# Kernel tuning notes

Hardware: AMD Instinct MI355X
Metric: run time of the kernel (lower is better)

## Reference

```python
import jax, jax.numpy as jnp
import numpy as np

STRIDES = [8, 16, 32, 64, 128]
SIZES = [32.0, 64.0, 128.0, 256.0, 512.0]
FEAT_HW = [(100, 152), (50, 76), (25, 38), (13, 19), (7, 10)]
N, C, A, K = 2, 256, 9, 80
SCORE_TH, TOPK, NMS_TH, MAX_DET = 0.05, 1000, 0.5, 100
IMG_H, IMG_W = 800.0, 1216.0
SCALE_CLAMP = float(np.log(1000.0 / 16.0))


def _cell_anchors(size):
    ratios = [0.5, 1.0, 2.0]
    scales = [2 ** 0, 2 ** (1.0 / 3), 2 ** (2.0 / 3)]
    out = []
    for s in scales:
        area = (size * s) ** 2
        for r in ratios:
            w = np.sqrt(area / r)
            h = w * r
            out.append([-w / 2.0, -h / 2.0, w / 2.0, h / 2.0])
    return np.asarray(out, np.float32)  # (9, 4)


def make_anchors():
    ancs = []
    for (H, W), st, sz in zip(FEAT_HW, STRIDES, SIZES):
        cell = _cell_anchors(sz)
        sx = np.arange(W, dtype=np.float32) * st
        sy = np.arange(H, dtype=np.float32) * st
        gx, gy = np.meshgrid(sx, sy)
        shifts = np.stack([gx.ravel(), gy.ravel(), gx.ravel(), gy.ravel()], 1)
        ancs.append((shifts[:, None, :] + cell[None, :, :]).reshape(-1, 4).astype(np.float32))
    return ancs


def setup_inputs() -> dict:
    key = jax.random.key(0)
    ks = jax.random.split(key, 10)
    inp = {}
    for i, (H, W) in enumerate(FEAT_HW):
        inp[f"feat{i}"] = jax.random.normal(ks[i], (N, C, H, W), jnp.float32)
    inp["cls_sub_w"] = jax.random.normal(ks[5], (4, C, C, 3, 3), jnp.float32) * 0.01
    inp["cls_sub_b"] = jnp.zeros((4, C), jnp.float32)
    inp["bbox_sub_w"] = jax.random.normal(ks[6], (4, C, C, 3, 3), jnp.float32) * 0.01
    inp["bbox_sub_b"] = jnp.zeros((4, C), jnp.float32)
    inp["cls_score_w"] = jax.random.normal(ks[7], (A * K, C, 3, 3), jnp.float32) * 0.1
    inp["cls_score_b"] = jnp.full((A * K,), float(-np.log((1 - 0.01) / 0.01)), jnp.float32)
    inp["bbox_pred_w"] = jax.random.normal(ks[8], (A * 4, C, 3, 3), jnp.float32) * 0.01
    inp["bbox_pred_b"] = jnp.zeros((A * 4,), jnp.float32)
    for i, a in enumerate(make_anchors()):
        inp[f"anc{i}"] = jnp.asarray(a)
    return inp


def conv3(x, w, b):
    y = jax.lax.conv_general_dilated(x, w, (1, 1), 'SAME',
                                     dimension_numbers=('NCHW', 'OIHW', 'NCHW'))
    return y + b[None, :, None, None]


def head_level(x, csw, csb, bsw, bsb, scw, scb, bpw, bpb):
    c = x
    r = x
    for i in range(4):
        c = jax.nn.relu(conv3(c, csw[i], csb[i]))
        r = jax.nn.relu(conv3(r, bsw[i], bsb[i]))
    return conv3(c, scw, scb), conv3(r, bpw, bpb)


def to_NHWA_K(t, k):
    n, _, h, w = t.shape
    return t.reshape(n, -1, k, h, w).transpose(0, 3, 4, 1, 2).reshape(n, -1, k)


def decode(deltas, anchors):
    wa = anchors[..., 2] - anchors[..., 0]
    ha = anchors[..., 3] - anchors[..., 1]
    xa = anchors[..., 0] + 0.5 * wa
    ya = anchors[..., 1] + 0.5 * ha
    dx, dy = deltas[..., 0], deltas[..., 1]
    dw = jnp.minimum(deltas[..., 2], SCALE_CLAMP)
    dh = jnp.minimum(deltas[..., 3], SCALE_CLAMP)
    cx = dx * wa + xa
    cy = dy * ha + ya
    w = jnp.exp(dw) * wa
    h = jnp.exp(dh) * ha
    return jnp.stack([cx - 0.5 * w, cy - 0.5 * h, cx + 0.5 * w, cy + 0.5 * h], -1)


def iou_vs_all(box, boxes):
    lt = jnp.maximum(box[:2], boxes[:, :2])
    rb = jnp.minimum(box[2:], boxes[:, 2:])
    wh = jnp.clip(rb - lt, 0.0)
    inter = wh[:, 0] * wh[:, 1]
    a1 = (box[2] - box[0]) * (box[3] - box[1])
    a2 = (boxes[:, 2] - boxes[:, 0]) * (boxes[:, 3] - boxes[:, 1])
    return inter / (a1 + a2 - inter + 1e-9)


def nms_image(boxes, scores, classes):
    # class-aware NMS via coordinate offset per class (batched_nms trick)
    off = classes.astype(boxes.dtype)[:, None] * 4096.0
    b = boxes + off

    def body(i, st):
        sc, bi, bs = st
        j = jnp.argmax(sc)
        s = sc[j]
        bi = bi.at[i].set(j)
        bs = bs.at[i].set(s)
        iou = iou_vs_all(b[j], b)
        sc = jnp.where(iou > NMS_TH, 0.0, sc).at[j].set(0.0)
        return (sc, bi, bs)

    bi0 = jnp.zeros((MAX_DET,), jnp.int32)
    bs0 = jnp.zeros((MAX_DET,), boxes.dtype)
    _, bi, bs = jax.lax.fori_loop(0, MAX_DET, body, (scores, bi0, bs0))
    return boxes[bi], bs, classes[bi]


def reference(feat0, feat1, feat2, feat3, feat4, cls_sub_w, cls_sub_b,
              bbox_sub_w, bbox_sub_b, cls_score_w, cls_score_b,
              bbox_pred_w, bbox_pred_b, anc0, anc1, anc2, anc3, anc4):
    feats = [feat0, feat1, feat2, feat3, feat4]
    ancs = [anc0, anc1, anc2, anc3, anc4]
    cand_b, cand_s, cand_c = [], [], []
    for f, anc in zip(feats, ancs):
        logits, deltas = head_level(f, cls_sub_w, cls_sub_b, bbox_sub_w, bbox_sub_b,
                                    cls_score_w, cls_score_b, bbox_pred_w, bbox_pred_b)
        cls = to_NHWA_K(logits, K)       # (N, HWA, K)
        reg = to_NHWA_K(deltas, 4)       # (N, HWA, 4)
        n, hwa, _ = reg.shape
        prob = jax.nn.sigmoid(cls.reshape(n, hwa * K))
        ntk = min(TOPK, hwa)             # d2: min(topk_candidates, box_reg_i.size(0))
        vals, idxs = jax.lax.top_k(prob, ntk)
        a_idx = idxs // K
        c_idx = idxs % K
        d = jnp.take_along_axis(reg, a_idx[..., None], axis=1)   # (N, ntk, 4)
        anc_sel = anc[a_idx]                                      # (N, ntk, 4)
        boxes = decode(d, anc_sel)
        boxes = jnp.stack([jnp.clip(boxes[..., 0], 0.0, IMG_W),
                           jnp.clip(boxes[..., 1], 0.0, IMG_H),
                           jnp.clip(boxes[..., 2], 0.0, IMG_W),
                           jnp.clip(boxes[..., 3], 0.0, IMG_H)], -1)
        scores = jnp.where(vals > SCORE_TH, vals, 0.0)  # score threshold (keep_idxs)
        cand_b.append(boxes)
        cand_s.append(scores)
        cand_c.append(c_idx)
    B = jnp.concatenate(cand_b, 1)
    S = jnp.concatenate(cand_s, 1)
    Cl = jnp.concatenate(cand_c, 1)
    det_boxes, det_scores, det_classes = jax.vmap(nms_image)(B, S, Cl)
    return det_boxes, det_scores, det_classes
```

## Files before the change

### kernel.cpp

```cpp
#include <hip/hip_runtime.h>
#include <math.h>

#define NIMG 2
#define NCAND 4630
#define MAXDET 100
#define IMG_W_F 1216.0f
#define IMG_H_F 800.0f
#define SCORE_THR 0.05f
#define NMS_THR 0.5f
#define SCALE_CLAMP_F 4.135166556742356f

typedef __attribute__((ext_vector_type(8))) _Float16 f16x8;
typedef __attribute__((ext_vector_type(16))) float f32x16;

#define WOFF_CLS_T(i) ((unsigned)(i) * 589824u)
#define WOFF_BBX_T(i) (2359296u + (unsigned)(i) * 589824u)
#define WOFF_CLS_H 4718592u
#define WOFF_BBX_H 6488064u

#define BUF_HALFS 10944000u
#define TK_SLOT_U32 139272
#define NSLOT 10

struct ConvTab {
  int cum[6];
  int H[5], W[5];
  unsigned actOff[5];
};
struct CvtTab {
  const float* f[5];
  int cumR[6];
  int H[5], W[5];
  unsigned actOff[5];
};
struct HeadTab {
  int cum[6];
  unsigned actOff[5];
  int H[5], W[5];
  int pOffL[5];
  int pStride[5];
  int rOffL[5];
};
struct TKTab {
  int pOff[NSLOT]; int M[NSLOT]; int kk[NSLOT]; int rBase[NSLOT]; int outBase[NSLOT];
  const float* anc[NSLOT];
};
struct PPTab {
  const float* src[10];
  unsigned dstOff[10];
  int Cout[10];
  int nCoF[10];
  int cum[11];
};
struct HaloTab {
  int cumPx[6];
  int Hp[5], Wp[5];
  unsigned actOff[5];
};

__global__ __launch_bounds__(256)
void prepack_k(_Float16* __restrict__ dst0, PPTab tb)
{
  int t0 = blockIdx.x * 256 + threadIdx.x;
  if (t0 >= tb.cum[10]) return;
  int r = 0;
  for (int i = 1; i < 10; ++i) if (t0 >= tb.cum[i]) r = i;
  const int t = t0 - tb.cum[r];
  const float* src = tb.src[r];
  _Float16* dst = dst0 + tb.dstOff[r];
  const int Cout = tb.Cout[r], nCoF = tb.nCoF[r];

  const int l = t & 63;
  const int rest = t >> 6;
  const int coF = rest % nCoF;
  const int tc = rest / nCoF;
  const int tap = tc >> 4;
  const int cb = tc & 15;
  const int co = coF * 32 + (l & 31);
  const int ciB = cb * 16 + (l >> 5) * 8;
#pragma unroll
  for (int j = 0; j < 8; ++j) {
    float v = 0.f;
    if (co < Cout) v = src[(size_t)(co * 256 + ciB + j) * 9 + tap];
    dst[(size_t)t * 8 + j] = (_Float16)v;
  }
}

__global__ __launch_bounds__(256)
void halo_k(_Float16* __restrict__ actBase, HaloTab tb)
{
  int t = blockIdx.x * 256 + threadIdx.x;
  if (t >= 4 * 16 * 2 * 1000) return;
  const int buf = t / 32000;
  int r = t - buf * 32000;
  const int cbimg = r / 1000;
  const int px = r - cbimg * 1000;
  const int cb = cbimg >> 1, img = cbimg & 1;
  int l = 0;
#pragma unroll
  for (int i = 1; i < 5; ++i) if (px >= tb.cumPx[i]) l = i;
  const int pxl = px - tb.cumPx[l];
  const int Hp = tb.Hp[l], Wp = tb.Wp[l];
  int hp, wp;
  if (pxl < Wp) { hp = 0; wp = pxl; }
  else if (pxl < 2 * Wp) { hp = Hp - 1; wp = pxl - Wp; }
  else { int q = pxl - 2 * Wp; hp = 1 + (q >> 1); wp = (q & 1) ? (Wp - 1) : 0; }
  const unsigned CBS = 2u * (unsigned)(Hp * Wp) * 16u;
  _Float16* a = actBase + (size_t)buf * BUF_HALFS + tb.actOff[l] +
                (unsigned)cb * CBS + ((unsigned)((img * Hp + hp) * Wp + wp)) * 16u;
  f16x8 z = {};
  *(f16x8*)(a) = z;
  *(f16x8*)(a + 8) = z;
}

__global__ __launch_bounds__(256)
void convert_k(_Float16* __restrict__ act, CvtTab tb)
{
  int bz = blockIdx.x;
  int l = 0;
#pragma unroll
  for (int i = 1; i < 5; ++i) if (bz >= tb.cumR[i]) l = i;
  const int h = bz - tb.cumR[l];
  const int n = blockIdx.y;
  const int H = tb.H[l], W = tb.W[l];
  const int Hp = H + 2, Wp = W + 2, HpWp = Hp * Wp;
  const unsigned CBS = 2u * (unsigned)HpWp * 16u;
  const float* x = tb.f[l];
  _Float16* a = act + tb.actOff[l];
  __shared__ float s[64][154];
  for (int c0 = 0; c0 < 256; c0 += 64) {
    for (int idx = threadIdx.x; idx < 64 * W; idx += 256) {
      int c = idx / W, w = idx - c * W;
      s[c][w] = x[((size_t)(n * 256 + c0 + c) * H + h) * W + w];
    }
    __syncthreads();
    for (int idx = threadIdx.x; idx < 4 * W; idx += 256) {
      int ch = idx / W, w = idx - ch * W;
      int cchunk = (c0 >> 4) + ch;
      unsigned base = (unsigned)cchunk * CBS +
                      ((unsigned)((n * Hp + h + 1) * Wp + (w + 1))) * 16u;
      f16x8 v0, v1;
#pragma unroll
      for (int j = 0; j < 8; ++j) {
        v0[j] = (_Float16)s[ch * 16 + j][w];
        v1[j] = (_Float16)s[ch * 16 + 8 + j][w];
      }
      *(f16x8*)(a + base) = v0;
      *(f16x8*)(a + base + 8) = v1;
    }
    __syncthreads();
  }
}

__device__ __forceinline__ void conv_core(
    const _Float16* __restrict__ in, const _Float16* __restrict__ w,
    int nCoF, int coF0, int Wp, unsigned CBS, const unsigned V0, const unsigned V1,
    unsigned lOff, f32x16& a00, f32x16& a01, f32x16& a10, f32x16& a11)
{
  const unsigned wTap = 16u * (unsigned)nCoF * 512u;
  for (int cb = 0; cb < 16; cb += 2) {
    const _Float16* aB0 = in + (unsigned)cb * CBS;
    const _Float16* aB1 = aB0 + CBS;
    const _Float16* wB0 = w + ((unsigned)cb * (unsigned)nCoF + (unsigned)coF0) * 512u;
    const _Float16* wB1 = wB0 + (unsigned)nCoF * 512u;
#pragma unroll
    for (int tap = 0; tap < 9; ++tap) {
      const unsigned to = ((unsigned)((tap / 3) * Wp + (tap % 3))) * 16u;
      const _Float16* wT0 = wB0 + (unsigned)tap * wTap;
      const _Float16* wT1 = wB1 + (unsigned)tap * wTap;
      f16x8 x0 = *(const f16x8*)(aB0 + to + V0);
      f16x8 x1 = *(const f16x8*)(aB0 + to + V1);
      f16x8 y0 = *(const f16x8*)(aB1 + to + V0);
      f16x8 y1 = *(const f16x8*)(aB1 + to + V1);
      f16x8 u0 = *(const f16x8*)(wT0 + lOff);
      f16x8 u1 = *(const f16x8*)(wT0 + 512u + lOff);
      f16x8 v0 = *(const f16x8*)(wT1 + lOff);
      f16x8 v1 = *(const f16x8*)(wT1 + 512u + lOff);
      a00 = __builtin_amdgcn_mfma_f32_32x32x16_f16(x0, u0, a00, 0, 0, 0);
      a01 = __builtin_amdgcn_mfma_f32_32x32x16_f16(x0, u1, a01, 0, 0, 0);
      a10 = __builtin_amdgcn_mfma_f32_32x32x16_f16(x1, u0, a10, 0, 0, 0);
      a11 = __builtin_amdgcn_mfma_f32_32x32x16_f16(x1, u1, a11, 0, 0, 0);
      a00 = __builtin_amdgcn_mfma_f32_32x32x16_f16(y0, v0, a00, 0, 0, 0);
      a01 = __builtin_amdgcn_mfma_f32_32x32x16_f16(y0, v1, a01, 0, 0, 0);
      a10 = __builtin_amdgcn_mfma_f32_32x32x16_f16(y1, v0, a10, 0, 0, 0);
      a11 = __builtin_amdgcn_mfma_f32_32x32x16_f16(y1, v1, a11, 0, 0, 0);
    }
  }
}

__global__ __launch_bounds__(256)
void tower_k(const _Float16* __restrict__ inA, const _Float16* __restrict__ inB,
             const _Float16* __restrict__ wpk,
             const float* __restrict__ biasA, const float* __restrict__ biasB,
             _Float16* __restrict__ outA, _Float16* __restrict__ outB,
             unsigned wOffA, unsigned wOffB, ConvTab tb)
{
  int bz = blockIdx.y;
  int l = 0;
#pragma unroll
  for (int i = 1; i < 5; ++i) if (bz >= tb.cum[i]) l = i;
  const int bx = bz - tb.cum[l];
  const int H = tb.H[l], W = tb.W[l];
  const int Wp = W + 2, HW = H * W, HpWp = (H + 2) * Wp;
  const unsigned CBS = 2u * (unsigned)HpWp * 16u;
  const int chain = blockIdx.x >> 1, cg2 = blockIdx.x & 1;
  const _Float16* in = (chain ? inB : inA) + tb.actOff[l];
  _Float16* out = (chain ? outB : outA) + tb.actOff[l];
  const _Float16* w = wpk + (chain ? wOffB : wOffA);
  const float* bias = chain ? biasB : biasA;
  const int Mloc = 2 * HW;

  const int wave = threadIdx.x >> 6;
  const int wr = wave & 1, wc = wave >> 1;
  const int lane = threadIdx.x & 63;
  const int lw = lane & 31;
  const int lh = lane >> 5;
  const int mBase = bx * 128 + wr * 64;
  const int coF0 = cg2 * 4 + wc * 2;
  unsigned V[2];
#pragma unroll
  for (int i = 0; i < 2; ++i) {
    int mloc = mBase + i * 32 + lw;
    if (mloc >= Mloc) mloc = Mloc - 1;
    int n = mloc / HW; int rem = mloc - n * HW;
    int h = rem / W; int ww = rem - h * W;
    V[i] = ((unsigned)(n * HpWp + h * Wp + ww)) * 16u + (unsigned)lh * 8u;
  }
  f32x16 a00 = {}, a01 = {}, a10 = {}, a11 = {};
  conv_core(in, w, 8, coF0, Wp, CBS, V[0], V[1], (unsigned)lane * 8u,
            a00, a01, a10, a11);

  const int coBase = coF0 * 32;
  const f32x16* accs[4] = {&a00, &a01, &a10, &a11};
#pragma unroll
  for (int q = 0; q < 4; ++q) {
    const f32x16& A = *accs[q];
    const int i = q >> 1, f = q & 1;
    const int co = coBase + f * 32 + lw;
    const float bv = bias[co];
#pragma unroll
    for (int r = 0; r < 16; ++r) {
      int mloc = mBase + i * 32 + ((r & 3) + 8 * (r >> 2) + 4 * lh);
      if (mloc >= Mloc) continue;
      int n = mloc / HW; int rem = mloc - n * HW;
      int h = rem / W; int ww = rem - h * W;
      unsigned addr = ((unsigned)(co >> 4)) * CBS +
                      ((unsigned)(n * HpWp + (h + 1) * Wp + (ww + 1))) * 16u +
                      (unsigned)(co & 15);
      out[addr] = (_Float16)fmaxf(A[r] + bv, 0.f);
    }
  }
}

__global__ __launch_bounds__(256)
void head_k(const _Float16* __restrict__ inC, const _Float16* __restrict__ inX,
            const _Float16* __restrict__ wpk,
            const float* __restrict__ scb, const float* __restrict__ bpb,
            float* __restrict__ P, _Float16* __restrict__ Rh, HeadTab tb)
{
  int bz = blockIdx.y;
  int li = 0;
#pragma unroll
  for (int i = 1; i < 5; ++i) if (bz >= tb.cum[i]) li = i;
  const int bx = bz - tb.cum[li];
  const int H = tb.H[li], W = tb.W[li];
  const int Wp = W + 2, HW = H * W, HpWp = (H + 2) * Wp;
  const unsigned CBS = 2u * (unsigned)HpWp * 16u;
  const int img = blockIdx.z;
  const int y = blockIdx.x;

  const int wave = threadIdx.x >> 6;
  const int wr = wave & 1, wc = wave >> 1;
  const int lane = threadIdx.x & 63;
  const int lw = lane & 31;
  const int lh = lane >> 5;

  const _Float16* in;
  const _Float16* w;
  const float* bias;
  int nCoF, coF0, Cout;
  if (y < 6) {
    in = inC + tb.actOff[li]; w = wpk + WOFF_CLS_H; bias = scb;
    nCoF = 24; coF0 = y * 4 + wc * 2; Cout = 720;
  } else {
    if (wc) return;
    in = inX + tb.actOff[li]; w = wpk + WOFF_BBX_H; bias = bpb;
    nCoF = 2; coF0 = 0; Cout = 36;
  }
  const int Mloc = HW;
  const int mBase = bx * 128 + wr * 64;
  unsigned V[2];
#pragma unroll
  for (int i = 0; i < 2; ++i) {
    int mloc = mBase + i * 32 + lw;
    if (mloc >= Mloc) mloc = Mloc - 1;
    int h = mloc / W; int ww = mloc - h * W;
    V[i] = ((unsigned)(img * HpWp + h * Wp + ww)) * 16u + (unsigned)lh * 8u;
  }
  f32x16 a00 = {}, a01 = {}, a10 = {}, a11 = {};
  conv_core(in, w, nCoF, coF0, Wp, CBS, V[0], V[1], (unsigned)lane * 8u,
            a00, a01, a10, a11);

  const long long pBase = (long long)tb.pOffL[li] +
                          (long long)img * (long long)tb.pStride[li];
  const size_t rBase = (size_t)tb.rOffL[li] + (size_t)img * HW * 36;
  const int coBase = coF0 * 32;
  const f32x16* accs[4] = {&a00, &a01, &a10, &a11};
#pragma unroll
  for (int q = 0; q < 4; ++q) {
    const f32x16& A = *accs[q];
    const int i = q >> 1, f = q & 1;
    const int co = coBase + f * 32 + lw;
    const float bv = (co < Cout) ? bias[co] : 0.f;
#pragma unroll
    for (int r = 0; r < 16; ++r) {
      int mloc = mBase + i * 32 + ((r & 3) + 8 * (r >> 2) + 4 * lh);
      if (mloc >= Mloc) continue;
      float v = A[r] + bv;
      if (y < 6) {
        if (co < 720) P[pBase + (long long)mloc * 720 + co] = 1.f / (1.f + expf(-v));
      } else {
        if (co < 36) Rh[rBase + (size_t)mloc * 36 + co] = (_Float16)v;
      }
    }
  }
}

__global__ __launch_bounds__(256)
void hist_coarse_k(const float* __restrict__ wsF, unsigned* __restrict__ tkbuf, TKTab t)
{
  const int slot = blockIdx.y;
  __shared__ unsigned lh[8192];
  for (int i = threadIdx.x; i < 8192; i += 256) lh[i] = 0;
  __syncthreads();
  const float* p = wsF + t.pOff[slot];
  const int M = t.M[slot];
  for (int i = blockIdx.x * 256 + threadIdx.x; i < M; i += gridDim.x * 256)
    atomicAdd(&lh[(__float_as_uint(p[i]) >> 17) & 8191u], 1u);
  __syncthreads();
  unsigned* h = tkbuf + (size_t)slot * TK_SLOT_U32;
  for (int i = threadIdx.x; i < 8192; i += 256) {
    unsigned c = lh[i];
    if (c) atomicAdd(&h[i], c);
  }
}

__global__ __launch_bounds__(256)
void hist_fine_k(const float* __restrict__ wsF, unsigned* __restrict__ tkbuf, TKTab t)
{
  const int slot = blockIdx.y;
  unsigned* base = tkbuf + (size_t)slot * TK_SLOT_U32;
  const unsigned cb = base[8192 + 131072 + 0];
  const float* p = wsF + t.pOff[slot];
  const int M = t.M[slot];
  unsigned* h = base + 8192;
  for (int i = blockIdx.x * 256 + threadIdx.x; i < M; i += gridDim.x * 256) {
    unsigned b = __float_as_uint(p[i]);
    if ((b >> 17) == cb) atomicAdd(&h[b & 0x1FFFFu], 1u);
  }
}

__global__ __launch_bounds__(1024)
void radix_scan_k(unsigned* __restrict__ tkbuf, TKTab t, int phase)
{
  const int slot = blockIdx.x;
  unsigned* base = tkbuf + (size_t)slot * TK_SLOT_U32;
  const unsigned* hb0 = base + (phase ? 8192 : 0);
  unsigned* s = base + 8192 + 131072;
  const int nbins = phase ? 131072 : 8192;
  const int k = t.kk[slot];
  const int per = nbins / 1024;
  const int tid = threadIdx.x;
  const unsigned* hb = hb0 + tid * per;
  unsigned local = 0;
  for (int i = 0; i < per; ++i) local += hb[i];
  __shared__ unsigned part[1024];
  part[tid] = local;
  __syncthreads();
  for (int d = 1; d < 1024; d <<= 1) {
    unsigned v = (tid + d < 1024) ? part[tid + d] : 0u;
    __syncthreads();
    part[tid] += v;
    __syncthreads();
  }
  unsigned above = part[tid] - local;
  unsigned kk = (phase == 0) ? (unsigned)k : ((unsigned)k - s[1]);
  if (above < kk && above + local >= kk) {
    unsigned cum = above;
    for (int i = per - 1; i >= 0; --i) {
      unsigned c = hb[i];
      if (cum + c >= kk) {
        if (phase == 0) { s[0] = (unsigned)(tid * per + i); s[1] = cum; }
        else { s[2] = (s[0] << 17) | (unsigned)(tid * per + i); s[4] = kk - cum; }
        break;
      }
      cum += c;
    }
  }
}

__global__ __launch_bounds__(256)
void compact_k(const float* __restrict__ wsF, unsigned* __restrict__ tkbuf,
               float* __restrict__ cv, unsigned* __restrict__ ci,
               unsigned* __restrict__ eq, TKTab t)
{
  const int slot = blockIdx.y;
  unsigned* s = tkbuf + (size_t)slot * TK_SLOT_U32 + 8192 + 131072;
  const unsigned thr = s[2];
  const float* p = wsF + t.pOff[slot];
  const int M = t.M[slot];
  float* cvn = cv + slot * 1024;
  unsigned* cin_ = ci + slot * 1024;
  unsigned* eqn = eq + (size_t)slot * 8192;
  for (int i = blockIdx.x * 256 + threadIdx.x; i < M; i += gridDim.x * 256) {
    unsigned b = __float_as_uint(p[i]);
    if (b > thr) {
      unsigned g = atomicAdd(&s[5], 1u);
      if (g < 1024u) { cvn[g] = p[i]; cin_[g] = (unsigned)i; }
    } else if (b == thr) {
      unsigned e = atomicAdd(&s[6], 1u);
      if (e < 8192u) eqn[e] = (unsigned)i;
    }
  }
}

__global__ __launch_bounds__(1024)
void finalize_k(const float* __restrict__ cv, const unsigned* __restrict__ ci,
                const unsigned* __restrict__ eq, const unsigned* __restrict__ tkbuf,
                const _Float16* __restrict__ Rh, TKTab t,
                float* __restrict__ candB, float* __restrict__ candS, float* __restrict__ candC)
{
  const int slot = blockIdx.x;
  const int tid = threadIdx.x;
  const unsigned* s = tkbuf + (size_t)slot * TK_SLOT_U32 + 8192 + 131072;
  const float* anc = t.anc[slot];
  const int k = t.kk[slot];
  __shared__ float svals[1024];
  __shared__ unsigned sidx[1024];
  __shared__ unsigned long long key[1024];
  const unsigned cntG = s[5] < 1024u ? s[5] : 1024u;
  const unsigned nEq = s[4];
  if (tid < (int)cntG) {
    svals[tid] = cv[slot * 1024 + tid];
    sidx[tid] = ci[slot * 1024 + tid];
  }
  __syncthreads();
  if (tid == 0) {
    unsigned cnt = s[6] < 8192u ? s[6] : 8192u;
    unsigned last = 0; int first = 1;
    float tv = __uint_as_float(s[2]);
    for (unsigned e2 = 0; e2 < nEq && cntG + e2 < 1024u; ++e2) {
      unsigned best = 0xFFFFFFFFu;
      for (unsigned q = 0; q < cnt; ++q) {
        unsigned v = eq[(size_t)slot * 8192 + q];
        if ((first || v > last) && v < best) best = v;
      }
      svals[cntG + e2] = tv; sidx[cntG + e2] = best;
      last = best; first = 0;
    }
  }
  __syncthreads();
  const int kk = (int)cntG + (int)nEq;
  key[tid] = (tid < kk)
      ? (((unsigned long long)__float_as_uint(svals[tid]) << 32) |
         (unsigned long long)(0xFFFFFFFFu - sidx[tid]))
      : 0ULL;
  __syncthreads();
  for (int sz = 2; sz <= 1024; sz <<= 1) {
    for (int st = sz >> 1; st > 0; st >>= 1) {
      int ixj = tid ^ st;
      if (ixj > tid) {
        unsigned long long a = key[tid], b = key[ixj];
        bool up = ((tid & sz) == 0);
        if (up ? (a < b) : (a > b)) { key[tid] = b; key[ixj] = a; }
      }
      __syncthreads();
    }
  }
  if (tid < kk && tid < k) {
    unsigned long long kv = key[tid];
    float val = __uint_as_float((unsigned)(kv >> 32));
    unsigned idx = 0xFFFFFFFFu - (unsigned)(kv & 0xFFFFFFFFu);
    unsigned a = idx / 80u;
    unsigned cls = idx - a * 80u;
    const _Float16* rg = Rh + (size_t)t.rBase[slot] + (size_t)a * 4;
    float a0 = anc[(size_t)a * 4 + 0], a1 = anc[(size_t)a * 4 + 1];
    float a2 = anc[(size_t)a * 4 + 2], a3 = anc[(size_t)a * 4 + 3];
    float wa = a2 - a0, ha = a3 - a1;
    float xa = a0 + 0.5f * wa, ya = a1 + 0.5f * ha;
    float dx = (float)rg[0], dy = (float)rg[1];
    float dw = fminf((float)rg[2], SCALE_CLAMP_F), dh = fminf((float)rg[3], SCALE_CLAMP_F);
    float cx = dx * wa + xa, cy = dy * ha + ya;
    float wb = expf(dw) * wa, hb = expf(dh) * ha;
    float x0 = cx - 0.5f * wb, y0 = cy - 0.5f * hb;
    float x1 = cx + 0.5f * wb, y1 = cy + 0.5f * hb;
    x0 = fminf(fmaxf(x0, 0.f), IMG_W_F);
    y0 = fminf(fmaxf(y0, 0.f), IMG_H_F);
    x1 = fminf(fmaxf(x1, 0.f), IMG_W_F);
    y1 = fminf(fmaxf(y1, 0.f), IMG_H_F);
    int o = t.outBase[slot] + tid;
    candB[(size_t)o * 4 + 0] = x0; candB[(size_t)o * 4 + 1] = y0;
    candB[(size_t)o * 4 + 2] = x1; candB[(size_t)o * 4 + 3] = y1;
    candS[o] = (val > SCORE_THR) ? val : 0.f;
    candC[o] = (float)cls;
  }
}

__global__ __launch_bounds__(1024)
void nms_k(const float* __restrict__ cB, const float* __restrict__ cS,
           const float* __restrict__ cC, float* __restrict__ out)
{
  const int n = blockIdx.x;
  const int tid = threadIdx.x;
  const int wid = tid >> 6, lane = tid & 63;
  __shared__ float S[NCAND];
  __shared__ float wv_[16];
  __shared__ int wi_[16];
  __shared__ float bj[5];
  __shared__ int sjs;
  for (int i = tid; i < NCAND; i += 1024) S[i] = cS[n * NCAND + i];
  __syncthreads();
  for (int it = 0; it < MAXDET; ++it) {
    float bv = -1.f; int bix = 0;
    for (int i = tid; i < NCAND; i += 1024) {
      float v = S[i];
      if (v > bv) { bv = v; bix = i; }
    }
#pragma unroll
    for (int d = 32; d > 0; d >>= 1) {
      float v2 = __shfl_down(bv, d);
      int i2 = __shfl_down(bix, d);
      if (v2 > bv || (v2 == bv && i2 < bix)) { bv = v2; bix = i2; }
    }
    if (lane == 0) { wv_[wid] = bv; wi_[wid] = bix; }
    __syncthreads();
    if (tid < 64) {
      float v = (tid < 16) ? wv_[tid] : -2.f;
      int ix = (tid < 16) ? wi_[tid] : 0x7FFFFFFF;
#pragma unroll
      for (int d = 8; d > 0; d >>= 1) {
        float v2 = __shfl_down(v, d);
        int i2 = __shfl_down(ix, d);
        if (v2 > v || (v2 == v && i2 < ix)) { v = v2; ix = i2; }
      }
      if (tid == 0) {
        bj[4] = v; sjs = ix;
        if (v > 0.f) {
          const int j = ix;
          float b0 = cB[(size_t)(n * NCAND + j) * 4 + 0];
          float b1 = cB[(size_t)(n * NCAND + j) * 4 + 1];
          float b2 = cB[(size_t)(n * NCAND + j) * 4 + 2];
          float b3 = cB[(size_t)(n * NCAND + j) * 4 + 3];
          out[((size_t)n * MAXDET + it) * 4 + 0] = b0;
          out[((size_t)n * MAXDET + it) * 4 + 1] = b1;
          out[((size_t)n * MAXDET + it) * 4 + 2] = b2;
          out[((size_t)n * MAXDET + it) * 4 + 3] = b3;
          out[800 + n * MAXDET + it] = v;
          out[1000 + n * MAXDET + it] = cC[n * NCAND + j];
          float off = cC[n * NCAND + j] * 4096.f;
          bj[0] = b0 + off; bj[1] = b1 + off; bj[2] = b2 + off; bj[3] = b3 + off;
        }
      }
    }
    __syncthreads();
    const float mv = bj[4];
    const int j = sjs;
    if (mv <= 0.f) {
      float b0 = cB[(size_t)(n * NCAND) * 4 + 0], b1 = cB[(size_t)(n * NCAND) * 4 + 1];
      float b2 = cB[(size_t)(n * NCAND) * 4 + 2], b3 = cB[(size_t)(n * NCAND) * 4 + 3];
      float c0 = cC[n * NCAND];
      for (int t2 = it + tid; t2 < MAXDET; t2 += 1024) {
        out[((size_t)n * MAXDET + t2) * 4 + 0] = b0;
        out[((size_t)n * MAXDET + t2) * 4 + 1] = b1;
        out[((size_t)n * MAXDET + t2) * 4 + 2] = b2;
        out[((size_t)n * MAXDET + t2) * 4 + 3] = b3;
        out[800 + n * MAXDET + t2] = 0.f;
        out[1000 + n * MAXDET + t2] = c0;
      }
      return;
    }
    const float jx0 = bj[0], jy0 = bj[1], jx1 = bj[2], jy1 = bj[3];
    const float aj = (jx1 - jx0) * (jy1 - jy0);
    for (int i = tid; i < NCAND; i += 1024) {
      if (i == j) { S[i] = 0.f; continue; }
      if (S[i] == 0.f) continue;
      float off = cC[n * NCAND + i] * 4096.f;
      float x0 = cB[(size_t)(n * NCAND + i) * 4 + 0] + off;
      float y0 = cB[(size_t)(n * NCAND + i) * 4 + 1] + off;
      float x1 = cB[(size_t)(n * NCAND + i) * 4 + 2] + off;
      float y1 = cB[(size_t)(n * NCAND + i) * 4 + 3] + off;
      float lx = fmaxf(jx0, x0), ly = fmaxf(jy0, y0);
      float rx = fminf(jx1, x1), ry = fminf(jy1, y1);
      float iw = fmaxf(rx - lx, 0.f), ih = fmaxf(ry - ly, 0.f);
      float inter = iw * ih;
      float ai = (x1 - x0) * (y1 - y0);
      float iou = inter / (aj + ai - inter + 1e-9f);
      if (iou > NMS_THR) S[i] = 0.f;
    }
    __syncthreads();
  }
}

extern "C" void kernel_launch(void* const* d_in, const int* in_sizes, int n_in,
                              void* d_out, int out_size, void* d_ws, size_t ws_size,
                              hipStream_t stream)
{
  static const int LH[5] = {100, 50, 25, 13, 7};
  static const int LW[5] = {152, 76, 38, 19, 10};
  static const int LHW[5] = {15200, 3800, 950, 247, 70};
  static const int NTK[5] = {1000, 1000, 1000, 1000, 630};
  static const int OFFS[5] = {0, 1000, 2000, 3000, 4000};
  static const unsigned ACTOFF[5] = {0u, 8042496u, 10119168u, 10672128u, 10833408u};
  static const int CUMT128[6] = {0, 238, 298, 313, 317, 319};
  static const int CUMH128[6] = {0, 119, 149, 157, 159, 160};
  static const int CUMR[6] = {0, 100, 150, 175, 188, 195};
  static const int ROFF[5] = {0, 1094400, 1368000, 1436400, 1454184};
  static const int POFF14[4] = {0, 2736000, 3420000, 3597840};

  const float* feat[5]; const float* anc[5];
  for (int l = 0; l < 5; ++l) {
    feat[l] = (const float*)d_in[l];
    anc[l] = (const float*)d_in[13 + l];
  }
  const float* csw = (const float*)d_in[5];
  const float* csb = (const float*)d_in[6];
  const float* bsw = (const float*)d_in[7];
  const float* bsb = (const float*)d_in[8];
  const float* scw = (const float*)d_in[9];
  const float* scb = (const float*)d_in[10];
  const float* bpw = (const float*)d_in[11];
  const float* bpb = (const float*)d_in[12];

  float* wsF = (float*)d_ws;
  size_t o = 0;
  _Float16* actBase = (_Float16*)(wsF + o); o += (size_t)4 * BUF_HALFS / 2;
  _Float16* wpk = (_Float16*)(wsF + o); o += 3317760;
  float* P0 = wsF + o; o += 10944000;
  _Float16* Rh = (_Float16*)(wsF + o); o += 729612;
  float* candB = wsF + o; o += (size_t)NIMG * NCAND * 4;
  float* candS = wsF + o; o += NIMG * NCAND;
  float* candC = wsF + o; o += NIMG * NCAND;
  float* candV = wsF + o; o += NSLOT * 1024;
  unsigned* candI = (unsigned*)(wsF + o); o += NSLOT * 1024;
  unsigned* eqI = (unsigned*)(wsF + o); o += NSLOT * 8192;
  unsigned* tkbuf = (unsigned*)(wsF + o); o += (size_t)NSLOT * TK_SLOT_U32;
  if (ws_size < o * sizeof(float)) return;

  _Float16* X = actBase;
  _Float16* A = X + BUF_HALFS;
  _Float16* B = A + BUF_HALFS;
  _Float16* C = B + BUF_HALFS;
  float* P1 = (float*)A;
  const int PX_L14_IMG0 = 0;
  const int PC_L14_IMG1 = 16416000;
  float* out = (float*)d_out;

  {
    PPTab pp;
    static const int PPC[11] = {0, 73728, 147456, 221184, 294912, 368640,
                                442368, 516096, 589824, 811008, 829440};
    for (int i = 0; i < 11; ++i) pp.cum[i] = PPC[i];
    for (int i = 0; i < 4; ++i) {
      pp.src[i] = csw + (size_t)i * 589824; pp.dstOff[i] = WOFF_CLS_T(i);
      pp.Cout[i] = 256; pp.nCoF[i] = 8;
      pp.src[4 + i] = bsw + (size_t)i * 589824; pp.dstOff[4 + i] = WOFF_BBX_T(i);
      pp.Cout[4 + i] = 256; pp.nCoF[4 + i] = 8;
    }
    pp.src[8] = scw; pp.dstOff[8] = WOFF_CLS_H; pp.Cout[8] = 720; pp.nCoF[8] = 24;
    pp.src[9] = bpw; pp.dstOff[9] = WOFF_BBX_H; pp.Cout[9] = 36; pp.nCoF[9] = 2;
    prepack_k<<<dim3(3240), dim3(256), 0, stream>>>(wpk, pp);
  }

  {
    HaloTab hzt;
    static const int HCUM[6] = {0, 508, 764, 894, 962, 1000};
    for (int i = 0; i < 6; ++i) hzt.cumPx[i] = HCUM[i];
    for (int l = 0; l < 5; ++l) {
      hzt.Hp[l] = LH[l] + 2; hzt.Wp[l] = LW[l] + 2; hzt.actOff[l] = ACTOFF[l];
    }
    halo_k<<<dim3((128000 + 255) / 256), dim3(256), 0, stream>>>(X, hzt);
  }

  ConvTab ct;
  CvtTab vt;
  for (int l = 0; l < 5; ++l) {
    ct.H[l] = LH[l]; ct.W[l] = LW[l]; ct.actOff[l] = ACTOFF[l];
    vt.f[l] = feat[l]; vt.H[l] = LH[l]; vt.W[l] = LW[l]; vt.actOff[l] = ACTOFF[l];
  }
  for (int i = 0; i < 6; ++i) { ct.cum[i] = CUMT128[i]; vt.cumR[i] = CUMR[i]; }

  convert_k<<<dim3(195, NIMG), dim3(256), 0, stream>>>(X, vt);

  tower_k<<<dim3(4, 319), dim3(256), 0, stream>>>(X, X, wpk, csb + 0, bsb + 0, A, B,
      WOFF_CLS_T(0), WOFF_BBX_T(0), ct);
  tower_k<<<dim3(4, 319), dim3(256), 0, stream>>>(A, B, wpk, csb + 256, bsb + 256, C, X,
      WOFF_CLS_T(1), WOFF_BBX_T(1), ct);
  tower_k<<<dim3(4, 319), dim3(256), 0, stream>>>(C, X, wpk, csb + 512, bsb + 512, A, B,
      WOFF_CLS_T(2), WOFF_BBX_T(2), ct);
  tower_k<<<dim3(4, 319), dim3(256), 0, stream>>>(A, B, wpk, csb + 768, bsb + 768, C, X,
      WOFF_CLS_T(3), WOFF_BBX_T(3), ct);

  const int p0Off = (int)(P0 - wsF);
  const int p1Off = (int)(P1 - wsF);

  {
    HeadTab ht = {};
    ht.cum[0] = 0; ht.cum[1] = 119;
    for (int i = 2; i < 6; ++i) ht.cum[i] = 0x7FFFFFFF;
    ht.actOff[0] = ACTOFF[0]; ht.H[0] = LH[0]; ht.W[0] = LW[0];
    ht.pOffL[0] = p0Off; ht.pStride[0] = p1Off - p0Off;
    ht.rOffL[0] = ROFF[0];
    head_k<<<dim3(7, 119, 2), dim3(256), 0, stream>>>(C, X, wpk, scb, bpb, wsF, Rh, ht);
  }
  {
    HeadTab ht = {};
    static const int CUMH14[6] = {0, 30, 38, 40, 41, 0x7FFFFFFF};
    for (int i = 0; i < 6; ++i) ht.cum[i] = CUMH14[i];
    for (int i = 0; i < 4; ++i) {
      int l = i + 1;
      ht.actOff[i] = ACTOFF[l]; ht.H[i] = LH[l]; ht.W[i] = LW[l];
      ht.pOffL[i] = PX_L14_IMG0 + POFF14[i];
      ht.pStride[i] = PC_L14_IMG1 - PX_L14_IMG0;
      ht.rOffL[i] = ROFF[l];
    }
    head_k<<<dim3(7, 41, 2), dim3(256), 0, stream>>>(C, X, wpk, scb, bpb, wsF, Rh, ht);
  }

  {
    TKTab tk = {};
    tk.pOff[0] = p0Off; tk.pOff[1] = p1Off;
    for (int img = 0; img < 2; ++img) {
      tk.M[img] = LHW[0] * 720; tk.kk[img] = NTK[0];
      tk.rBase[img] = ROFF[0] + img * LHW[0] * 36;
      tk.outBase[img] = img * NCAND + OFFS[0];
      tk.anc[img] = anc[0];
    }
    for (int s = 2; s < 10; ++s) {
      int i = s - 2;
      int l = (i & 3) + 1, img = i >> 2;
      tk.pOff[s] = (img ? PC_L14_IMG1 : PX_L14_IMG0) + POFF14[l - 1];
      tk.M[s] = LHW[l] * 720;
      tk.kk[s] = NTK[l];
      tk.rBase[s] = ROFF[l] + img * LHW[l] * 36;
      tk.outBase[s] = img * NCAND + OFFS[l];
      tk.anc[s] = anc[l];
    }
    hipMemsetAsync(tkbuf, 0, (size_t)NSLOT * TK_SLOT_U32 * 4, stream);
    hist_coarse_k<<<dim3(256, NSLOT), dim3(256), 0, stream>>>(wsF, tkbuf, tk);
    radix_scan_k<<<dim3(NSLOT), dim3(1024), 0, stream>>>(tkbuf, tk, 0);
    hist_fine_k<<<dim3(256, NSLOT), dim3(256), 0, stream>>>(wsF, tkbuf, tk);
    radix_scan_k<<<dim3(NSLOT), dim3(1024), 0, stream>>>(tkbuf, tk, 1);
    compact_k<<<dim3(256, NSLOT), dim3(256), 0, stream>>>(wsF, tkbuf, candV, candI, eqI, tk);
    finalize_k<<<dim3(NSLOT), dim3(1024), 0, stream>>>(candV, candI, eqI, tkbuf, Rh, tk,
                                                       candB, candS, candC);
  }
  nms_k<<<dim3(NIMG), dim3(1024), 0, stream>>>(candB, candS, candC, out);
}
```

Baseline: 1.340 ms.

## Store class probabilities as fp16 and run radix top-k on 16-bit keys

The head kernel now writes sigmoid probabilities as fp16 instead of fp32, halving the largest intermediate write. The histogram, scan, compact and finalize top-k stages are reworked to use 16-bit keys: 4096 coarse bins and 65536 fine bins, with correspondingly smaller scratch slots and memset. The intent is to cut memory traffic in the head output and in the repeated top-k passes. The cost is reduced score precision, so many more candidates tie at the threshold value, which may change which entries are selected and makes the tie list more likely to overflow.

```diff
diff --git a/kernel.cpp b/kernel.cpp
--- a/kernel.cpp
+++ b/kernel.cpp
@@ -19,7 +19,7 @@
 #define WOFF_BBX_H 6488064u
 
 #define BUF_HALFS 10944000u
-#define TK_SLOT_U32 139272
+#define TK_SLOT_U32 69640
 #define NSLOT 10
 
 struct ConvTab {
@@ -37,12 +37,13 @@
   int cum[6];
   unsigned actOff[5];
   int H[5], W[5];
-  int pOffL[5];
-  int pStride[5];
+  long long pOffL[5];
+  long long pStride[5];
   int rOffL[5];
 };
 struct TKTab {
-  int pOff[NSLOT]; int M[NSLOT]; int kk[NSLOT]; int rBase[NSLOT]; int outBase[NSLOT];
+  long long pOff[NSLOT];
+  int M[NSLOT]; int kk[NSLOT]; int rBase[NSLOT]; int outBase[NSLOT];
   const float* anc[NSLOT];
 };
 struct PPTab {
@@ -57,6 +58,13 @@
   int Hp[5], Wp[5];
   unsigned actOff[5];
 };
+
+__device__ __forceinline__ unsigned short f16bits(_Float16 h) {
+  union { _Float16 h; unsigned short u; } c; c.h = h; return c.u;
+}
+__device__ __forceinline__ float f16tof(unsigned short u) {
+  union { unsigned short u; _Float16 h; } c; c.u = u; return (float)c.h;
+}
 
 __global__ __launch_bounds__(256)
 void prepack_k(_Float16* __restrict__ dst0, PPTab tb)
@@ -256,7 +264,7 @@
 void head_k(const _Float16* __restrict__ inC, const _Float16* __restrict__ inX,
             const _Float16* __restrict__ wpk,
             const float* __restrict__ scb, const float* __restrict__ bpb,
-            float* __restrict__ P, _Float16* __restrict__ Rh, HeadTab tb)
+            _Float16* __restrict__ PH, _Float16* __restrict__ Rh, HeadTab tb)
 {
   int bz = blockIdx.y;
   int li = 0;
@@ -301,8 +309,7 @@
   conv_core(in, w, nCoF, coF0, Wp, CBS, V[0], V[1], (unsigned)lane * 8u,
             a00, a01, a10, a11);
 
-  const long long pBase = (long long)tb.pOffL[li] +
-                          (long long)img * (long long)tb.pStride[li];
+  const long long pBase = tb.pOffL[li] + (long long)img * tb.pStride[li];
   const size_t rBase = (size_t)tb.rOffL[li] + (size_t)img * HW * 36;
   const int coBase = coF0 * 32;
   const f32x16* accs[4] = {&a00, &a01, &a10, &a11};
@@ -318,7 +325,8 @@
       if (mloc >= Mloc) continue;
       float v = A[r] + bv;
       if (y < 6) {
-        if (co < 720) P[pBase + (long long)mloc * 720 + co] = 1.f / (1.f + expf(-v));
+        if (co < 720)
+          PH[pBase + (long long)mloc * 720 + co] = (_Float16)(1.f / (1.f + expf(-v)));
       } else {
         if (co < 36) Rh[rBase + (size_t)mloc * 36 + co] = (_Float16)v;
       }
@@ -327,36 +335,36 @@
 }
 
 __global__ __launch_bounds__(256)
-void hist_coarse_k(const float* __restrict__ wsF, unsigned* __restrict__ tkbuf, TKTab t)
+void hist_coarse_k(const _Float16* __restrict__ PH, unsigned* __restrict__ tkbuf, TKTab t)
 {
   const int slot = blockIdx.y;
-  __shared__ unsigned lh[8192];
-  for (int i = threadIdx.x; i < 8192; i += 256) lh[i] = 0;
+  __shared__ unsigned lh[4096];
+  for (int i = threadIdx.x; i < 4096; i += 256) lh[i] = 0;
   __syncthreads();
-  const float* p = wsF + t.pOff[slot];
+  const _Float16* p = PH + t.pOff[slot];
   const int M = t.M[slot];
   for (int i = blockIdx.x * 256 + threadIdx.x; i < M; i += gridDim.x * 256)
-    atomicAdd(&lh[(__float_as_uint(p[i]) >> 17) & 8191u], 1u);
+    atomicAdd(&lh[f16bits(p[i]) >> 4], 1u);
   __syncthreads();
   unsigned* h = tkbuf + (size_t)slot * TK_SLOT_U32;
-  for (int i = threadIdx.x; i < 8192; i += 256) {
+  for (int i = threadIdx.x; i < 4096; i += 256) {
     unsigned c = lh[i];
     if (c) atomicAdd(&h[i], c);
   }
 }
 
 __global__ __launch_bounds__(256)
-void hist_fine_k(const float* __restrict__ wsF, unsigned* __restrict__ tkbuf, TKTab t)
+void hist_fine_k(const _Float16* __restrict__ PH, unsigned* __restrict__ tkbuf, TKTab t)
 {
   const int slot = blockIdx.y;
   unsigned* base = tkbuf + (size_t)slot * TK_SLOT_U32;
-  const unsigned cb = base[8192 + 131072 + 0];
-  const float* p = wsF + t.pOff[slot];
+  const unsigned cb = base[4096 + 65536 + 0];
+  const _Float16* p = PH + t.pOff[slot];
   const int M = t.M[slot];
-  unsigned* h = base + 8192;
+  unsigned* h = base + 4096;
   for (int i = blockIdx.x * 256 + threadIdx.x; i < M; i += gridDim.x * 256) {
-    unsigned b = __float_as_uint(p[i]);
-    if ((b >> 17) == cb) atomicAdd(&h[b & 0x1FFFFu], 1u);
+    unsigned b = f16bits(p[i]);
+    if ((b >> 4) == cb) atomicAdd(&h[b], 1u);
   }
 }
 
@@ -365,9 +373,9 @@
 {
   const int slot = blockIdx.x;
   unsigned* base = tkbuf + (size_t)slot * TK_SLOT_U32;
-  const unsigned* hb0 = base + (phase ? 8192 : 0);
-  unsigned* s = base + 8192 + 131072;
-  const int nbins = phase ? 131072 : 8192;
+  const unsigned* hb0 = base + (phase ? 4096 : 0);
+  unsigned* s = base + 4096 + 65536;
+  const int nbins = phase ? 65536 : 4096;
   const int k = t.kk[slot];
   const int per = nbins / 1024;
   const int tid = threadIdx.x;
@@ -391,7 +399,7 @@
       unsigned c = hb[i];
       if (cum + c >= kk) {
         if (phase == 0) { s[0] = (unsigned)(tid * per + i); s[1] = cum; }
-        else { s[2] = (s[0] << 17) | (unsigned)(tid * per + i); s[4] = kk - cum; }
+        else { s[2] = (unsigned)(tid * per + i); s[4] = kk - cum; }
         break;
       }
       cum += c;
@@ -400,23 +408,23 @@
 }
 
 __global__ __launch_bounds__(256)
-void compact_k(const float* __restrict__ wsF, unsigned* __restrict__ tkbuf,
+void compact_k(const _Float16* __restrict__ PH, unsigned* __restrict__ tkbuf,
                float* __restrict__ cv, unsigned* __restrict__ ci,
                unsigned* __restrict__ eq, TKTab t)
 {
   const int slot = blockIdx.y;
-  unsigned* s = tkbuf + (size_t)slot * TK_SLOT_U32 + 8192 + 131072;
+  unsigned* s = tkbuf + (size_t)slot * TK_SLOT_U32 + 4096 + 65536;
   const unsigned thr = s[2];
-  const float* p = wsF + t.pOff[slot];
+  const _Float16* p = PH + t.pOff[slot];
   const int M = t.M[slot];
   float* cvn = cv + slot * 1024;
   unsigned* cin_ = ci + slot * 1024;
   unsigned* eqn = eq + (size_t)slot * 8192;
   for (int i = blockIdx.x * 256 + threadIdx.x; i < M; i += gridDim.x * 256) {
-    unsigned b = __float_as_uint(p[i]);
+    unsigned b = f16bits(p[i]);
     if (b > thr) {
       unsigned g = atomicAdd(&s[5], 1u);
-      if (g < 1024u) { cvn[g] = p[i]; cin_[g] = (unsigned)i; }
+      if (g < 1024u) { cvn[g] = (float)p[i]; cin_[g] = (unsigned)i; }
     } else if (b == thr) {
       unsigned e = atomicAdd(&s[6], 1u);
       if (e < 8192u) eqn[e] = (unsigned)i;
@@ -432,7 +440,7 @@
 {
   const int slot = blockIdx.x;
   const int tid = threadIdx.x;
-  const unsigned* s = tkbuf + (size_t)slot * TK_SLOT_U32 + 8192 + 131072;
+  const unsigned* s = tkbuf + (size_t)slot * TK_SLOT_U32 + 4096 + 65536;
   const float* anc = t.anc[slot];
   const int k = t.kk[slot];
   __shared__ float svals[1024];
@@ -448,7 +456,7 @@
   if (tid == 0) {
     unsigned cnt = s[6] < 8192u ? s[6] : 8192u;
     unsigned last = 0; int first = 1;
-    float tv = __uint_as_float(s[2]);
+    float tv = f16tof((unsigned short)s[2]);
     for (unsigned e2 = 0; e2 < nEq && cntG + e2 < 1024u; ++e2) {
       unsigned best = 0xFFFFFFFFu;
       for (unsigned q = 0; q < cnt; ++q) {
@@ -612,7 +620,6 @@
   static const int OFFS[5] = {0, 1000, 2000, 3000, 4000};
   static const unsigned ACTOFF[5] = {0u, 8042496u, 10119168u, 10672128u, 10833408u};
   static const int CUMT128[6] = {0, 238, 298, 313, 317, 319};
-  static const int CUMH128[6] = {0, 119, 149, 157, 159, 160};
   static const int CUMR[6] = {0, 100, 150, 175, 188, 195};
   static const int ROFF[5] = {0, 1094400, 1368000, 1436400, 1454184};
   static const int POFF14[4] = {0, 2736000, 3420000, 3597840};
@@ -650,10 +657,12 @@
   _Float16* A = X + BUF_HALFS;
   _Float16* B = A + BUF_HALFS;
   _Float16* C = B + BUF_HALFS;
-  float* P1 = (float*)A;
-  const int PX_L14_IMG0 = 0;
-  const int PC_L14_IMG1 = 16416000;
+  _Float16* PH = actBase;
   float* out = (float*)d_out;
+
+  const long long P0H = (long long)((_Float16*)P0 - PH);
+  const long long PXH = 0;
+  const long long PCH = 3LL * BUF_HALFS;
 
   {
     PPTab pp;
@@ -700,17 +709,14 @@
   tower_k<<<dim3(4, 319), dim3(256), 0, stream>>>(A, B, wpk, csb + 768, bsb + 768, C, X,
       WOFF_CLS_T(3), WOFF_BBX_T(3), ct);
 
-  const int p0Off = (int)(P0 - wsF);
-  const int p1Off = (int)(P1 - wsF);
-
   {
     HeadTab ht = {};
     ht.cum[0] = 0; ht.cum[1] = 119;
     for (int i = 2; i < 6; ++i) ht.cum[i] = 0x7FFFFFFF;
     ht.actOff[0] = ACTOFF[0]; ht.H[0] = LH[0]; ht.W[0] = LW[0];
-    ht.pOffL[0] = p0Off; ht.pStride[0] = p1Off - p0Off;
+    ht.pOffL[0] = P0H; ht.pStride[0] = (long long)BUF_HALFS;
     ht.rOffL[0] = ROFF[0];
-    head_k<<<dim3(7, 119, 2), dim3(256), 0, stream>>>(C, X, wpk, scb, bpb, wsF, Rh, ht);
+    head_k<<<dim3(7, 119, 2), dim3(256), 0, stream>>>(C, X, wpk, scb, bpb, PH, Rh, ht);
   }
   {
     HeadTab ht = {};
@@ -719,16 +725,16 @@
     for (int i = 0; i < 4; ++i) {
       int l = i + 1;
       ht.actOff[i] = ACTOFF[l]; ht.H[i] = LH[l]; ht.W[i] = LW[l];
-      ht.pOffL[i] = PX_L14_IMG0 + POFF14[i];
-      ht.pStride[i] = PC_L14_IMG1 - PX_L14_IMG0;
+      ht.pOffL[i] = PXH + POFF14[i];
+      ht.pStride[i] = PCH - PXH;
       ht.rOffL[i] = ROFF[l];
     }
-    head_k<<<dim3(7, 41, 2), dim3(256), 0, stream>>>(C, X, wpk, scb, bpb, wsF, Rh, ht);
+    head_k<<<dim3(7, 41, 2), dim3(256), 0, stream>>>(C, X, wpk, scb, bpb, PH, Rh, ht);
   }
 
   {
     TKTab tk = {};
-    tk.pOff[0] = p0Off; tk.pOff[1] = p1Off;
+    tk.pOff[0] = P0H; tk.pOff[1] = P0H + (long long)BUF_HALFS;
     for (int img = 0; img < 2; ++img) {
       tk.M[img] = LHW[0] * 720; tk.kk[img] = NTK[0];
       tk.rBase[img] = ROFF[0] + img * LHW[0] * 36;
@@ -738,7 +744,7 @@
     for (int s = 2; s < 10; ++s) {
       int i = s - 2;
       int l = (i & 3) + 1, img = i >> 2;
-      tk.pOff[s] = (img ? PC_L14_IMG1 : PX_L14_IMG0) + POFF14[l - 1];
+      tk.pOff[s] = (img ? PCH : PXH) + POFF14[l - 1];
       tk.M[s] = LHW[l] * 720;
       tk.kk[s] = NTK[l];
       tk.rBase[s] = ROFF[l] + img * LHW[l] * 36;
@@ -746,11 +752,11 @@
       tk.anc[s] = anc[l];
     }
     hipMemsetAsync(tkbuf, 0, (size_t)NSLOT * TK_SLOT_U32 * 4, stream);
-    hist_coarse_k<<<dim3(256, NSLOT), dim3(256), 0, stream>>>(wsF, tkbuf, tk);
+    hist_coarse_k<<<dim3(256, NSLOT), dim3(256), 0, stream>>>(PH, tkbuf, tk);
     radix_scan_k<<<dim3(NSLOT), dim3(1024), 0, stream>>>(tkbuf, tk, 0);
-    hist_fine_k<<<dim3(256, NSLOT), dim3(256), 0, stream>>>(wsF, tkbuf, tk);
+    hist_fine_k<<<dim3(256, NSLOT), dim3(256), 0, stream>>>(PH, tkbuf, tk);
     radix_scan_k<<<dim3(NSLOT), dim3(1024), 0, stream>>>(tkbuf, tk, 1);
-    compact_k<<<dim3(256, NSLOT), dim3(256), 0, stream>>>(wsF, tkbuf, candV, candI, eqI, tk);
+    compact_k<<<dim3(256, NSLOT), dim3(256), 0, stream>>>(PH, tkbuf, candV, candI, eqI, tk);
     finalize_k<<<dim3(NSLOT), dim3(1024), 0, stream>>>(candV, candI, eqI, tkbuf, Rh, tk,
                                                        candB, candS, candC);
   }
```

Result: slower. 1.419 ms (+5.9%).
